# Kernel tuning notes

Measured on AMD Instinct MI355X. Metric: run time of the kernel, lower is better.

## Reference

```python
import jax, jax.numpy as jnp
import numpy as np

IN_DIM, HID, MID, FFN, OUT = 384, 128, 1024, 512, 1024
B, T = 8, 4096
LN_EPS = 1e-5


def _legs_hippo(n: int) -> np.ndarray:
    # A[i, j] = P_i(2j/n - 1) * sqrt(2i + 1), Legendre via 3-term recurrence
    x = 2.0 * np.arange(n) / n - 1.0          # eval points, shape [n]
    P = np.zeros((n, n), dtype=np.float64)     # P[i] = P_i(x)
    P[0] = 1.0
    if n > 1:
        P[1] = x
    for i in range(1, n - 1):
        P[i + 1] = ((2 * i + 1) * x * P[i] - i * P[i - 1]) / (i + 1)
    A = P * np.sqrt(2.0 * np.arange(n) + 1.0)[:, None]
    # rescale so the 4096-step recurrence stays finite (A is a free Parameter,
    # so any test value is valid; unscaled LegS overflows fp32 in ~20 steps)
    s = np.linalg.norm(A, 2)
    return (A / (1.05 * s)).astype(np.float32)


def _layernorm(x, g, b):
    mu = jnp.mean(x, axis=-1, keepdims=True)
    var = jnp.var(x, axis=-1, keepdims=True)
    return (x - mu) * jax.lax.rsqrt(var + LN_EPS) * g + b


def setup_inputs() -> dict:
    key = jax.random.key(0)
    ks = jax.random.split(key, 16)

    def w(k, shape, fan_in):
        return jax.random.normal(k, shape, jnp.float32) * (1.0 / np.sqrt(fan_in))

    return {
        "padded_x": jax.random.normal(ks[0], (B, T, IN_DIM), jnp.float32),
        "seq_lens": jax.random.randint(ks[1], (B,), 1, T + 1, jnp.int32),
        "A": jnp.asarray(_legs_hippo(HID)),
        "enc_w1": w(ks[2], (IN_DIM, MID), IN_DIM), "enc_b1": jnp.zeros((MID,), jnp.float32),
        "enc_w2": w(ks[3], (MID, HID), MID), "enc_b2": jnp.zeros((HID,), jnp.float32),
        "proj_w": w(ks[4], (HID, MID), HID), "proj_b": jnp.zeros((MID,), jnp.float32),
        "ln1_g": jnp.ones((MID,), jnp.float32), "ln1_b": jnp.zeros((MID,), jnp.float32),
        "ffn_w1": w(ks[5], (MID, FFN), MID), "ffn_b1": jnp.zeros((FFN,), jnp.float32),
        "ffn_w2": w(ks[6], (FFN, OUT), FFN), "ffn_b2": jnp.zeros((OUT,), jnp.float32),
        "ln2_g": jnp.ones((OUT,), jnp.float32), "ln2_b": jnp.zeros((OUT,), jnp.float32),
        "out_w": w(ks[7], (OUT, OUT), OUT), "out_b": jnp.zeros((OUT,), jnp.float32),
    }


def reference(padded_x, seq_lens, A, enc_w1, enc_b1, enc_w2, enc_b2,
              proj_w, proj_b, ln1_g, ln1_b, ffn_w1, ffn_b1, ffn_w2, ffn_b2,
              ln2_g, ln2_b, out_w, out_b):
    # encoder: Linear -> GELU(exact) -> Linear   [B, T, HID]
    h_mid = jax.nn.gelu(padded_x @ enc_w1 + enc_b1, approximate=False)
    seqs_bx = h_mid @ enc_w2 + enc_b2

    # masked linear recurrence h_t = A @ h_{t-1} + Bx_t via lax.scan over time
    xs = jnp.swapaxes(seqs_bx, 0, 1)           # [T, B, HID]
    ts = jnp.arange(xs.shape[0])

    def step(h, inp):
        x_t, t = inp
        upd = h @ A.T + x_t                     # (A @ h)^T batched
        mask = (t < seq_lens)[:, None]          # [B, 1]
        return jnp.where(mask, upd, h), None

    h0 = jnp.zeros((padded_x.shape[0], A.shape[0]), padded_x.dtype)
    batch_h, _ = jax.lax.scan(step, h0, (xs, ts))

    # decoder
    projected = batch_h @ proj_w + proj_b
    norm_h = _layernorm(projected, ln1_g, ln1_b)
    ffn_out = jax.nn.gelu(norm_h @ ffn_w1 + ffn_b1, approximate=False) @ ffn_w2 + ffn_b2
    ffn_out = ffn_out + projected               # residual (requires OUT == MID)
    norm_ffn = _layernorm(ffn_out, ln2_g, ln2_b)
    return norm_ffn @ out_w + out_b             # [B, OUT]
```

## Files before the change

kernel.cpp:

```cpp
#include <hip/hip_runtime.h>

typedef __attribute__((ext_vector_type(8))) short short8;
typedef __attribute__((ext_vector_type(4))) short short4v;
typedef __attribute__((ext_vector_type(4))) float float4v;

__device__ __forceinline__ float bf2f(short s) {
  union { float f; unsigned u; } cv; cv.u = ((unsigned)(unsigned short)s) << 16; return cv.f;
}
__device__ __forceinline__ short f2bf(float f) {
  union { float f; unsigned u; } cv; cv.f = f;
  unsigned u = cv.u;
  unsigned r = u + 0x7FFFu + ((u >> 16) & 1u);
  return (short)(r >> 16);
}
__device__ __forceinline__ float gelu_f(float v) {
  float ax = fabsf(v) * 0.70710678118654752440f;
  float t = __builtin_amdgcn_rcpf(__builtin_fmaf(0.3275911f, ax, 1.0f));
  float poly = __builtin_fmaf(t, 1.061405429f, -1.453152027f);
  poly = __builtin_fmaf(t, poly, 1.421413741f);
  poly = __builtin_fmaf(t, poly, -0.284496736f);
  poly = __builtin_fmaf(t, poly, 0.254829592f);
  poly *= t;
  float e = __expf(-ax * ax);
  float erfax = __builtin_fmaf(-poly, e, 1.0f);
  float erfx = (v < 0.0f) ? -erfax : erfax;
  return 0.5f * v * (1.0f + erfx);
}
__device__ __forceinline__ void glds16(const short* g, short* l) {
  __builtin_amdgcn_global_load_lds(
      (const __attribute__((address_space(1))) void*)g,
      (__attribute__((address_space(3))) void*)l, 16, 0, 0);
}

__device__ __forceinline__ void mm128(const short* __restrict__ P, const short* __restrict__ Qt,
                                      int mode, short* __restrict__ R,
                                      int table1, int slot,
                                      short* __restrict__ P1, short* __restrict__ P1t,
                                      short* __restrict__ P2t)
{
  int t = threadIdx.x, lane = t & 63, wave = t >> 6;
  int l15 = lane & 15, quad = lane >> 4;
#pragma unroll 1
  for (int p = 0; p < 2; ++p) {
    float4v acc[8];
#pragma unroll
    for (int nt = 0; nt < 8; ++nt) acc[nt] = 0;
#pragma unroll 1
    for (int ks = 0; ks < 4; ++ks) {
      short8 af = *(const short8*)&P[(wave * 32 + p * 16 + l15) * 128 + ks * 32 + quad * 8];
#pragma unroll
      for (int nt = 0; nt < 8; ++nt) {
        short8 bf = *(const short8*)&Qt[(nt * 16 + l15) * 128 + ks * 32 + quad * 8];
        acc[nt] = __builtin_amdgcn_mfma_f32_16x16x32_bf16(af, bf, acc[nt], 0, 0, 0);
      }
    }
    int mb = wave * 32 + p * 16 + quad * 4;
#pragma unroll
    for (int nt = 0; nt < 8; ++nt) {
      int n = nt * 16 + l15;
      short4v o;
#pragma unroll
      for (int reg = 0; reg < 4; ++reg) o[reg] = f2bf(acc[nt][reg]);
      if (mode == 2) {
        if (table1) {
#pragma unroll
          for (int reg = 0; reg < 4; ++reg) P1[(size_t)(mb + reg) * 8192 + slot * 128 + n] = o[reg];
          *(short4v*)&P1t[((size_t)slot * 128 + n) * 128 + mb] = o;
        } else {
          *(short4v*)&P2t[((size_t)slot * 128 + n) * 128 + mb] = o;
        }
      } else {
#pragma unroll
        for (int reg = 0; reg < 4; ++reg) R[(mb + reg) * 128 + n] = o[reg];
      }
    }
  }
  __syncthreads();
}

__global__ __launch_bounds__(256) void enc_fused(
    const short* __restrict__ xB, const short* __restrict__ w1T,
    const short* __restrict__ w2T, const float* __restrict__ b1,
    float* __restrict__ encP, const int* __restrict__ seq_lens,
    short* __restrict__ Spow, short* __restrict__ SpowT)
{
  __shared__ __align__(16) short lds[20480];
  int tid = threadIdx.x, lane = tid & 63, wave = tid >> 6;
  int l15 = lane & 15, quad = lane >> 4;

  if (blockIdx.x >= 512) {
    if (blockIdx.x != 512 || blockIdx.y != 0) return;
    short* XTl = lds;
    for (int i = tid * 8; i < 16384; i += 2048) {
      short8 v = *(const short8*)&SpowT[i];
      int row = i >> 7, seg = (i & 127) >> 3;
      int sw = (seg & 8) | ((seg & 7) ^ (row & 7));
      *(short8*)&XTl[row * 128 + sw * 8] = v;
    }
    __syncthreads();
    for (int step = 1; step <= 11; ++step) {
      const short* gX = Spow + (size_t)(step - 1) * 16384;
      short* gXo  = Spow  + (size_t)step * 16384;
      short* gXTo = SpowT + (size_t)step * 16384;
      short4v outs[2][8];
#pragma unroll 1
      for (int p = 0; p < 2; ++p) {
        int row = wave * 32 + p * 16 + l15;
        short8 af[4];
#pragma unroll
        for (int ks = 0; ks < 4; ++ks)
          af[ks] = *(const short8*)&gX[row * 128 + ks * 32 + quad * 8];
        float4v acc[8];
#pragma unroll
        for (int nt = 0; nt < 8; ++nt) acc[nt] = 0;
#pragma unroll
        for (int ks = 0; ks < 4; ++ks) {
          int seg = ks * 4 + quad;
#pragma unroll
          for (int nt = 0; nt < 8; ++nt) {
            int br = nt * 16 + l15;
            int sw = (seg & 8) | ((seg & 7) ^ (br & 7));
            short8 bf = *(const short8*)&XTl[br * 128 + sw * 8];
            acc[nt] = __builtin_amdgcn_mfma_f32_16x16x32_bf16(af[ks], bf, acc[nt], 0, 0, 0);
          }
        }
        int mb = wave * 32 + p * 16 + quad * 4;
#pragma unroll
        for (int nt = 0; nt < 8; ++nt) {
          int n = nt * 16 + l15;
          short4v o;
#pragma unroll
          for (int reg = 0; reg < 4; ++reg) {
            o[reg] = f2bf(acc[nt][reg]);
            gXo[(mb + reg) * 128 + n] = o[reg];
          }
          *(short4v*)&gXTo[(size_t)n * 128 + mb] = o;
          outs[p][nt] = o;
        }
      }
      __syncthreads();
#pragma unroll
      for (int p = 0; p < 2; ++p) {
        int mb = wave * 32 + p * 16 + quad * 4;
#pragma unroll
        for (int nt = 0; nt < 8; ++nt) {
          int n = nt * 16 + l15;
          int seg = mb >> 3;
          int sw = (seg & 8) | ((seg & 7) ^ (n & 7));
          *(short4v*)&XTl[n * 128 + sw * 8 + (mb & 7)] = outs[p][nt];
        }
      }
      __syncthreads();
    }
    return;
  }

  int m0 = blockIdx.x * 64;
  { int b = m0 >> 12, t = m0 & 4095; if (t >= seq_lens[b]) return; }
  int nc0 = blockIdx.y * 2;

  short* As   = lds;
  short* Ws   = lds + 4096;
  short* midb = lds + 12288;

  int lr = lane >> 3, lseg = lane & 7;

  float4v accO[4][2];
#pragma unroll
  for (int i = 0; i < 4; i++)
#pragma unroll
    for (int j = 0; j < 2; j++) accO[i][j] = 0;

  for (int nci = 0; nci < 2; ++nci) {
    int nc = nc0 + nci;
    float4v accM[4][2];
#pragma unroll
    for (int i = 0; i < 4; i++)
#pragma unroll
      for (int j = 0; j < 2; j++) accM[i][j] = 0;

    for (int ks = 0; ks < 6; ++ks) {
      int kk = ks * 64;
#pragma unroll
      for (int i = 0; i < 2; i++) {
        int rowg = wave * 16 + i * 8;
        glds16(xB + (size_t)(m0 + rowg + lr) * 384 + kk + (lseg ^ lr) * 8, &As[rowg * 64]);
      }
#pragma unroll
      for (int i = 0; i < 4; i++) {
        int rowg = wave * 32 + i * 8;
        glds16(w1T + (size_t)(nc * 128 + rowg + lr) * 384 + kk + (lseg ^ lr) * 8, &Ws[rowg * 64]);
      }
      __syncthreads();
#pragma unroll
      for (int kh = 0; kh < 2; kh++) {
        int s = kh * 4 + quad;
        short8 af[4], bfr[2];
#pragma unroll
        for (int im = 0; im < 4; im++) {
          int r = im * 16 + l15;
          af[im] = *(short8*)&As[r * 64 + ((s ^ (r & 7)) * 8)];
        }
#pragma unroll
        for (int in = 0; in < 2; in++) {
          int r = wave * 32 + in * 16 + l15;
          bfr[in] = *(short8*)&Ws[r * 64 + ((s ^ (r & 7)) * 8)];
        }
#pragma unroll
        for (int im = 0; im < 4; im++)
#pragma unroll
          for (int in = 0; in < 2; in++)
            accM[im][in] = __builtin_amdgcn_mfma_f32_16x16x32_bf16(af[im], bfr[in], accM[im][in], 0, 0, 0);
      }
      __syncthreads();
    }
#pragma unroll
    for (int in = 0; in < 2; in++) {
      int k = wave * 32 + in * 16 + l15;
      float bias = b1[nc * 128 + k];
      int s = k >> 3, kb = k & 7;
#pragma unroll
      for (int im = 0; im < 4; im++)
#pragma unroll
        for (int reg = 0; reg < 4; reg++) {
          int m = im * 16 + quad * 4 + reg;
          float v = gelu_f(accM[im][in][reg] + bias);
          int sw = (s & 8) | ((s & 7) ^ (m & 7));
          midb[m * 128 + sw * 8 + kb] = f2bf(v);
        }
    }
    __syncthreads();
#pragma unroll
    for (int ks2 = 0; ks2 < 2; ++ks2) {
      int kk = nc * 128 + ks2 * 64;
#pragma unroll
      for (int i = 0; i < 4; i++) {
        int rowg = wave * 32 + i * 8;
        glds16(w2T + (size_t)(rowg + lr) * 1024 + kk + (lseg ^ lr) * 8, &Ws[rowg * 64]);
      }
      __syncthreads();
#pragma unroll
      for (int kh = 0; kh < 2; kh++) {
        short8 af[4], bfr[2];
#pragma unroll
        for (int im = 0; im < 4; im++) {
          int m = im * 16 + l15;
          int kb = ks2 * 64 + kh * 32 + quad * 8;
          int s = kb >> 3;
          int sw = (s & 8) | ((s & 7) ^ (m & 7));
          af[im] = *(short8*)&midb[m * 128 + sw * 8];
        }
#pragma unroll
        for (int in = 0; in < 2; in++) {
          int r = wave * 32 + in * 16 + l15;
          int s = kh * 4 + quad;
          bfr[in] = *(short8*)&Ws[r * 64 + ((s ^ (r & 7)) * 8)];
        }
#pragma unroll
        for (int im = 0; im < 4; im++)
#pragma unroll
          for (int in = 0; in < 2; in++)
            accO[im][in] = __builtin_amdgcn_mfma_f32_16x16x32_bf16(af[im], bfr[in], accO[im][in], 0, 0, 0);
      }
      __syncthreads();
    }
  }
  float* outp = encP + ((size_t)blockIdx.y << 22);
#pragma unroll
  for (int im = 0; im < 4; im++)
#pragma unroll
    for (int in = 0; in < 2; in++) {
      int n = wave * 32 + in * 16 + l15;
#pragma unroll
      for (int reg = 0; reg < 4; reg++) {
        int m = m0 + im * 16 + quad * 4 + reg;
        outp[(size_t)m * 128 + n] = accO[im][in][reg];
      }
    }
}

__global__ __launch_bounds__(256) void enc_reduce(
    const float* __restrict__ encP, const float* __restrict__ b2,
    short* __restrict__ seqs, const int* __restrict__ seq_lens,
    const short* __restrict__ Spow, const short* __restrict__ SpowT,
    short* __restrict__ P1, short* __restrict__ P1t, short* __restrict__ P2t,
    short* __restrict__ powScr)
{
  if (blockIdx.x >= 512) {
    int bid = blockIdx.x - 512;
    int table1 = bid < 63 ? 1 : 0;
    int e = table1 ? bid + 1 : bid - 62;
    int slot = 63 - e;
    int bits = e;
    int k0 = __ffs(bits) - 1; bits &= bits - 1;
    int s0 = table1 ? k0 : (k0 == 0 ? 6 : 6 + k0);
    const short* cur = Spow + (size_t)s0 * 16384;
    short* scr = powScr + (size_t)bid * 2 * 16384;
    int sb = 0;
    if (!bits) {
      int t = threadIdx.x;
      for (int idx = t * 8; idx < 16384; idx += 2048) {
        short8 v = *(const short8*)&cur[idx];
        int i = idx >> 7, j0 = idx & 127;
        if (table1) {
          *(short8*)&P1[(size_t)i * 8192 + slot * 128 + j0] = v;
#pragma unroll
          for (int q = 0; q < 8; ++q) P1t[((size_t)slot * 128 + j0 + q) * 128 + i] = v[q];
        } else {
#pragma unroll
          for (int q = 0; q < 8; ++q) P2t[((size_t)slot * 128 + j0 + q) * 128 + i] = v[q];
        }
      }
      return;
    }
    while (true) {
      int k = __ffs(bits) - 1; bits &= bits - 1;
      int si = table1 ? k : (k == 0 ? 6 : 6 + k);
      const short* Bt = SpowT + (size_t)si * 16384;
      if (!bits) {
        mm128(cur, Bt, 2, nullptr, table1, slot, P1, P1t, P2t);
        return;
      }
      mm128(cur, Bt, 1, scr + sb * 16384, 0, 0, nullptr, nullptr, nullptr);
      cur = scr + sb * 16384; sb ^= 1;
    }
  }

  int m0 = blockIdx.x * 64;
  { int b = m0 >> 12, t = m0 & 4095; if (t >= seq_lens[b]) return; }
  int t = threadIdx.x;
#pragma unroll
  for (int i = 0; i < 8; i++) {
    int f4 = t + i * 256;
    int m = m0 + (f4 >> 5);
    int cg = f4 & 31;
    size_t off = (size_t)m * 128 + cg * 4;
    float4v v = *(const float4v*)&encP[off];
#pragma unroll
    for (int y = 1; y < 4; y++) {
      float4v w = *(const float4v*)&encP[((size_t)y << 22) + off];
#pragma unroll
      for (int q = 0; q < 4; q++) v[q] += w[q];
    }
    float4v bb = *(const float4v*)&b2[cg * 4];
    short4v o;
#pragma unroll
    for (int q = 0; q < 4; q++) o[q] = f2bf(v[q] + bb[q]);
    *(short4v*)&seqs[off] = o;
  }
}

__global__ __launch_bounds__(256) void gemm_bt(
    const short* __restrict__ A_, const short* __restrict__ BT,
    float* __restrict__ out, int lda, int ldb, int ldc,
    int kSteps, int kChunk)
{
  int m0 = blockIdx.y * 128;
  int n0 = blockIdx.x * 128;
  int kBase = blockIdx.z * kChunk;

  __shared__ __align__(16) short As[128 * 64];
  __shared__ __align__(16) short Bs[128 * 64];

  int tid = threadIdx.x;
  int lane = tid & 63, wave = tid >> 6;
  int l15 = lane & 15, quad = lane >> 4;
  int wm = wave & 1, wn = wave >> 1;
  int lr = lane >> 3, lseg = lane & 7;

  float4v acc[4][4];
#pragma unroll
  for (int i = 0; i < 4; i++)
#pragma unroll
    for (int j = 0; j < 4; j++) acc[i][j] = 0;

  for (int ks = 0; ks < kSteps; ++ks) {
    int kk = kBase + ks * 64;
#pragma unroll
    for (int i = 0; i < 4; i++) {
      int rowg = wave * 32 + i * 8;
      glds16(A_ + (size_t)(m0 + rowg + lr) * lda + kk + (lseg ^ lr) * 8, &As[rowg * 64]);
      glds16(BT + (size_t)(n0 + rowg + lr) * ldb + kk + (lseg ^ lr) * 8, &Bs[rowg * 64]);
    }
    __syncthreads();
#pragma unroll
    for (int kh = 0; kh < 2; kh++) {
      int s = kh * 4 + quad;
      short8 af[4], bfr[4];
#pragma unroll
      for (int im = 0; im < 4; im++) {
        int r = wm * 64 + im * 16 + l15;
        af[im] = *(short8*)&As[r * 64 + ((s ^ (r & 7)) * 8)];
      }
#pragma unroll
      for (int in = 0; in < 4; in++) {
        int r = wn * 64 + in * 16 + l15;
        bfr[in] = *(short8*)&Bs[r * 64 + ((s ^ (r & 7)) * 8)];
      }
#pragma unroll
      for (int im = 0; im < 4; im++)
#pragma unroll
        for (int in = 0; in < 4; in++)
          acc[im][in] = __builtin_amdgcn_mfma_f32_16x16x32_bf16(af[im], bfr[in], acc[im][in], 0, 0, 0);
    }
    __syncthreads();
  }
  float* outz = out + (size_t)blockIdx.z * 65536;
#pragma unroll
  for (int im = 0; im < 4; im++)
#pragma unroll
    for (int in = 0; in < 4; in++) {
      int n = n0 + wn * 64 + in * 16 + l15;
#pragma unroll
      for (int reg = 0; reg < 4; reg++) {
        int m = m0 + wm * 64 + im * 16 + quad * 4 + reg;
        outz[(size_t)m * ldc + n] = acc[im][in][reg];
      }
    }
}

__global__ void prep_wide(const float* __restrict__ x, const float* __restrict__ w1,
                          const float* __restrict__ w2,
                          const float* __restrict__ proj_w, const float* __restrict__ ffn_w1,
                          const float* __restrict__ ffn_w2, const float* __restrict__ out_w,
                          const float* __restrict__ A, const int* __restrict__ seq_lens,
                          short* __restrict__ xB,
                          short* __restrict__ w1T, short* __restrict__ w2T,
                          short* __restrict__ projB, short* __restrict__ ffn1B,
                          short* __restrict__ ffn2B, short* __restrict__ outB,
                          short* __restrict__ P1, short* __restrict__ P1t,
                          short* __restrict__ P2t,
                          short* __restrict__ Spow, short* __restrict__ SpowT)
{
  int idx = blockIdx.x * 256 + threadIdx.x;
  if (idx < 3145728) {
    int row = idx / 96;
    int t = row & 4095, b = row >> 12;
    if (t >= seq_lens[b]) return;
    float4v v = ((const float4v*)x)[idx];
    short4v o;
#pragma unroll
    for (int j = 0; j < 4; j++) o[j] = f2bf(v[j]);
    ((short4v*)xB)[idx] = o;
    return;
  }
  idx -= 3145728;
  if (idx < 393216) {
    int n = idx / 384, k = idx % 384;
    w1T[idx] = f2bf(w1[k * 1024 + n]);
    return;
  }
  idx -= 393216;
  if (idx < 131072) {
    int n = idx / 1024, k = idx % 1024;
    w2T[idx] = f2bf(w2[k * 128 + n]);
    return;
  }
  idx -= 131072;
  if (idx < 131072) { projB[idx] = f2bf(proj_w[idx]); return; }
  idx -= 131072;
  if (idx < 524288) { ffn1B[idx] = f2bf(ffn_w1[idx]); return; }
  idx -= 524288;
  if (idx < 524288) { ffn2B[idx] = f2bf(ffn_w2[idx]); return; }
  idx -= 524288;
  if (idx < 1048576) { outB[idx] = f2bf(out_w[idx]); return; }
  idx -= 1048576;
  if (idx < 16384) {
    int i = idx >> 7, j = idx & 127;
    short bidv = f2bf((i == j) ? 1.0f : 0.0f);
    P1[i * 8192 + 63 * 128 + j] = bidv;
    P1t[(63 * 128 + j) * 128 + i] = bidv;
    P2t[(63 * 128 + j) * 128 + i] = bidv;
    short ab = f2bf(A[idx]);
    Spow[idx] = ab;
    SpowT[(size_t)j * 128 + i] = ab;
  }
}

__global__ __launch_bounds__(256) void combine_gemm(
    const float* __restrict__ Vz, const short* __restrict__ seqs,
    const int* __restrict__ seq_lens,
    const short* __restrict__ P2t, const short* __restrict__ P1t,
    float* __restrict__ hFtail)
{
  __shared__ short X[256 * 8];
  int pp = blockIdx.x >> 5, ks = blockIdx.x & 31;
  int t = threadIdx.x;
  for (int e = t; e < 2048; e += 256) {
    int klocal = e >> 3, b = e & 7;
    int cp = ks * 2 + (klocal >> 7), i = klocal & 127;
    int L = seq_lens[b];
    if (pp == 0) {
      int F = L >> 6, sh = 64 - F;
      float v = 0.f;
      if (cp >= sh) {
        int row = (b * 64 + (cp - sh)) * 128 + i;
#pragma unroll
        for (int z = 0; z < 32; z++) v += Vz[(size_t)z * 65536 + row];
      }
      X[e] = f2bf(v);
    } else {
      int F = L >> 6, rr = L & 63, sh = 64 - rr;
      short s = 0;
      if (cp >= sh) s = seqs[((size_t)b * 4096 + F * 64 + (cp - sh)) * 128 + i];
      X[e] = s;
    }
  }
  __syncthreads();
  const short* P = pp ? P1t : P2t;
  float* outp = hFtail + pp * 1024;
  int i = t & 127, g = t >> 7;
  float acc[4] = {0, 0, 0, 0};
  for (int kl = 0; kl < 256; ++kl) {
    int k = ks * 256 + kl;
    float pv = bf2f(P[k * 128 + i]);
    short4v xv = *(const short4v*)(X + kl * 8 + g * 4);
#pragma unroll
    for (int q = 0; q < 4; q++) acc[q] += bf2f(xv[q]) * pv;
  }
#pragma unroll
  for (int q = 0; q < 4; q++) atomicAdd(&outp[(g * 4 + q) * 128 + i], acc[q]);
}

__global__ __launch_bounds__(256) void proj_stage(
    const float* __restrict__ hFtail, const short* __restrict__ P1t,
    const int* __restrict__ seq_lens, const short* __restrict__ projB,
    const float* __restrict__ proj_b, float* __restrict__ projected)
{
  __shared__ short hT[128 * 8];
  __shared__ float red[4][64][8];
  int t = threadIdx.x;
  {
    int b = t >> 5, i4 = (t & 31) * 4;
    int rr = seq_lens[b] & 63;
    const short* M = P1t + (size_t)(63 - rr) * 128 * 128;
    const float* hF = hFtail + b * 128;
    float acc[4];
#pragma unroll
    for (int q = 0; q < 4; q++) acc[q] = hFtail[1024 + b * 128 + i4 + q];
    for (int j = 0; j < 128; ++j) {
      float hv = hF[j];
      short4v mv = *(const short4v*)&M[j * 128 + i4];
#pragma unroll
      for (int q = 0; q < 4; q++) acc[q] += bf2f(mv[q]) * hv;
    }
#pragma unroll
    for (int q = 0; q < 4; q++) hT[(i4 + q) * 8 + b] = f2bf(acc[q]);
  }
  __syncthreads();
  int c = t & 63, sl = t >> 6;
  int n = blockIdx.x * 64 + c;
  float acc[8] = {0, 0, 0, 0, 0, 0, 0, 0};
  for (int k = sl * 32; k < sl * 32 + 32; ++k) {
    short8 xv = *(short8*)&hT[k * 8];
    float wv = bf2f(projB[k * 1024 + n]);
#pragma unroll
    for (int b = 0; b < 8; b++) acc[b] += bf2f(xv[b]) * wv;
  }
#pragma unroll
  for (int b = 0; b < 8; b++) red[sl][c][b] = acc[b];
  __syncthreads();
  if (sl == 0) {
#pragma unroll
    for (int s = 1; s < 4; s++)
#pragma unroll
      for (int b = 0; b < 8; b++) acc[b] += red[s][c][b];
    float bn = proj_b[n];
#pragma unroll
    for (int b = 0; b < 8; b++) projected[b * 1024 + n] = acc[b] + bn;
  }
}

__global__ __launch_bounds__(256) void ffn1_stage(
    const float* __restrict__ projected, const float* __restrict__ g1,
    const float* __restrict__ b1, const short* __restrict__ ffn1B,
    float* __restrict__ ffn1raw)
{
  __shared__ float part[8][32][2];
  __shared__ float stats[8][2];
  __shared__ short xT[256 * 8];
  __shared__ float red[4][64][8];
  int t = threadIdx.x;
  { int b = t >> 5, j0 = t & 31; float s = 0, q = 0;
    for (int k = j0 * 32; k < j0 * 32 + 32; ++k) { float v = projected[b * 1024 + k]; s += v; q += v * v; }
    part[b][j0][0] = s; part[b][j0][1] = q; }
  __syncthreads();
  if (t < 8) {
    float s = 0, q = 0;
    for (int j = 0; j < 32; j++) { s += part[t][j][0]; q += part[t][j][1]; }
    float mu = s * (1.0f / 1024.0f);
    float var = q * (1.0f / 1024.0f) - mu * mu;
    stats[t][0] = mu; stats[t][1] = rsqrtf(var + 1e-5f);
  }
  __syncthreads();
  int ky0 = blockIdx.y * 256;
  for (int idx = t; idx < 2048; idx += 256) {
    int kl = idx >> 3, b = idx & 7; int k = ky0 + kl;
    float v = (projected[b * 1024 + k] - stats[b][0]) * stats[b][1] * g1[k] + b1[k];
    xT[kl * 8 + b] = f2bf(v);
  }
  __syncthreads();
  int c = t & 63, sl = t >> 6;
  int n = blockIdx.x * 64 + c;
  float acc[8] = {0, 0, 0, 0, 0, 0, 0, 0};
  for (int kl = sl * 64; kl < sl * 64 + 64; ++kl) {
    short8 xv = *(short8*)&xT[kl * 8];
    float wv = bf2f(ffn1B[(size_t)(ky0 + kl) * 512 + n]);
#pragma unroll
    for (int b = 0; b < 8; b++) acc[b] += bf2f(xv[b]) * wv;
  }
#pragma unroll
  for (int b = 0; b < 8; b++) red[sl][c][b] = acc[b];
  __syncthreads();
  if (sl == 0) {
#pragma unroll
    for (int s = 1; s < 4; s++)
#pragma unroll
      for (int b = 0; b < 8; b++) acc[b] += red[s][c][b];
#pragma unroll
    for (int b = 0; b < 8; b++) atomicAdd(&ffn1raw[b * 512 + n], acc[b]);
  }
}

__global__ __launch_bounds__(256) void ffn2_stage(
    const float* __restrict__ ffn1raw, const float* __restrict__ fb1,
    const short* __restrict__ ffn2B, float* __restrict__ ffn2raw)
{
  __shared__ short xT[256 * 8];
  __shared__ float red[4][64][8];
  int t = threadIdx.x;
  int ky0 = blockIdx.y * 256;
  for (int idx = t; idx < 2048; idx += 256) {
    int kl = idx >> 3, b = idx & 7; int k = ky0 + kl;
    float v = gelu_f(ffn1raw[b * 512 + k] + fb1[k]);
    xT[kl * 8 + b] = f2bf(v);
  }
  __syncthreads();
  int c = t & 63, sl = t >> 6;
  int n = blockIdx.x * 64 + c;
  float acc[8] = {0, 0, 0, 0, 0, 0, 0, 0};
  for (int kl = sl * 64; kl < sl * 64 + 64; ++kl) {
    short8 xv = *(short8*)&xT[kl * 8];
    float wv = bf2f(ffn2B[(size_t)(ky0 + kl) * 1024 + n]);
#pragma unroll
    for (int b = 0; b < 8; b++) acc[b] += bf2f(xv[b]) * wv;
  }
#pragma unroll
  for (int b = 0; b < 8; b++) red[sl][c][b] = acc[b];
  __syncthreads();
  if (sl == 0) {
#pragma unroll
    for (int s = 1; s < 4; s++)
#pragma unroll
      for (int b = 0; b < 8; b++) acc[b] += red[s][c][b];
#pragma unroll
    for (int b = 0; b < 8; b++) atomicAdd(&ffn2raw[b * 1024 + n], acc[b]);
  }
}

__global__ __launch_bounds__(256) void out_stage(
    const float* __restrict__ ffn2raw, const float* __restrict__ fb2,
    const float* __restrict__ projected, const float* __restrict__ g2,
    const float* __restrict__ b2ln, const short* __restrict__ outB,
    const float* __restrict__ out_b, float* __restrict__ d_out)
{
  __shared__ float part[8][32][2];
  __shared__ float stats[8][2];
  __shared__ short xT[512 * 8];
  __shared__ float red[4][64][8];
  int t = threadIdx.x;
  { int b = t >> 5, j0 = t & 31; float s = 0, q = 0;
    for (int k = j0 * 32; k < j0 * 32 + 32; ++k) {
      float v = ffn2raw[b * 1024 + k] + fb2[k] + projected[b * 1024 + k];
      s += v; q += v * v;
    }
    part[b][j0][0] = s; part[b][j0][1] = q; }
  __syncthreads();
  if (t < 8) {
    float s = 0, q = 0;
    for (int j = 0; j < 32; j++) { s += part[t][j][0]; q += part[t][j][1]; }
    float mu = s * (1.0f / 1024.0f);
    float var = q * (1.0f / 1024.0f) - mu * mu;
    stats[t][0] = mu; stats[t][1] = rsqrtf(var + 1e-5f);
  }
  __syncthreads();
  int ky0 = blockIdx.y * 512;
  for (int idx = t; idx < 4096; idx += 256) {
    int kl = idx >> 3, b = idx & 7; int k = ky0 + kl;
    float v = ffn2raw[b * 1024 + k] + fb2[k] + projected[b * 1024 + k];
    v = (v - stats[b][0]) * stats[b][1] * g2[k] + b2ln[k];
    xT[kl * 8 + b] = f2bf(v);
  }
  __syncthreads();
  int c = t & 63, sl = t >> 6;
  int n = blockIdx.x * 64 + c;
  float acc[8] = {0, 0, 0, 0, 0, 0, 0, 0};
  for (int kl = sl * 128; kl < sl * 128 + 128; ++kl) {
    short8 xv = *(short8*)&xT[kl * 8];
    float wv = bf2f(outB[(size_t)(ky0 + kl) * 1024 + n]);
#pragma unroll
    for (int b = 0; b < 8; b++) acc[b] += bf2f(xv[b]) * wv;
  }
#pragma unroll
  for (int b = 0; b < 8; b++) red[sl][c][b] = acc[b];
  __syncthreads();
  if (sl == 0) {
#pragma unroll
    for (int s = 1; s < 4; s++)
#pragma unroll
      for (int b = 0; b < 8; b++) acc[b] += red[s][c][b];
    float bn = (blockIdx.y == 0) ? out_b[n] : 0.0f;
#pragma unroll
    for (int b = 0; b < 8; b++) atomicAdd(&d_out[b * 1024 + n], acc[b] + bn);
  }
}

extern "C" void kernel_launch(void* const* d_in, const int* in_sizes, int n_in,
                              void* d_out, int out_size, void* d_ws, size_t ws_size,
                              hipStream_t stream)
{
  (void)in_sizes; (void)n_in; (void)out_size; (void)ws_size;
  const float* x      = (const float*)d_in[0];
  const int* seq_lens = (const int*)d_in[1];
  const float* A      = (const float*)d_in[2];
  const float* enc_w1 = (const float*)d_in[3];
  const float* enc_b1 = (const float*)d_in[4];
  const float* enc_w2 = (const float*)d_in[5];
  const float* enc_b2 = (const float*)d_in[6];
  const float* proj_w = (const float*)d_in[7];
  const float* proj_b = (const float*)d_in[8];
  const float* ln1_g  = (const float*)d_in[9];
  const float* ln1_b  = (const float*)d_in[10];
  const float* ffn_w1 = (const float*)d_in[11];
  const float* ffn_b1 = (const float*)d_in[12];
  const float* ffn_w2 = (const float*)d_in[13];
  const float* ffn_b2 = (const float*)d_in[14];
  const float* ln2_g  = (const float*)d_in[15];
  const float* ln2_b  = (const float*)d_in[16];
  const float* out_w  = (const float*)d_in[17];
  const float* out_b  = (const float*)d_in[18];

  char* p = (char*)d_ws;
  auto alloc = [&](size_t bytes) { char* r = p; p += (bytes + 255) & ~(size_t)255; return r; };
  short* xB    = (short*)alloc(32768ull * 384 * 2);
  float* encP  = (float*)alloc(4ull * 32768 * 128 * 4);
  short* seqs  = (short*)alloc(32768ull * 128 * 2);
  short* w1T   = (short*)alloc(1024ull * 384 * 2);
  short* w2T   = (short*)alloc(128ull * 1024 * 2);
  short* projB = (short*)alloc(128ull * 1024 * 2);
  short* ffn1B = (short*)alloc(1024ull * 512 * 2);
  short* ffn2B = (short*)alloc(512ull * 1024 * 2);
  short* outB  = (short*)alloc(1024ull * 1024 * 2);
  short* Spow  = (short*)alloc(12ull * 16384 * 2);
  short* SpowT = (short*)alloc(12ull * 16384 * 2);
  short* P1    = (short*)alloc(128ull * 8192 * 2);
  short* P1t   = (short*)alloc(8192ull * 128 * 2);
  short* P2t   = (short*)alloc(8192ull * 128 * 2);
  short* powScr= (short*)alloc(126ull * 2 * 16384 * 2);
  float* Vz    = (float*)alloc(32ull * 512 * 128 * 4);
  float* hFtail  = (float*)alloc(2ull * 8 * 128 * 4);
  float* ffn1raw = (float*)alloc(8ull * 512 * 4);
  float* ffn2raw = (float*)alloc(8ull * 1024 * 4);
  float* projected = (float*)alloc(8ull * 1024 * 4);

  hipMemsetAsync(hFtail, 0, (2ull * 8 * 128 + 8ull * 512 + 8ull * 1024) * 4, stream);
  hipMemsetAsync(d_out, 0, 8192ull * 4, stream);

  prep_wide<<<23104, 256, 0, stream>>>(x, enc_w1, enc_w2, proj_w, ffn_w1, ffn_w2, out_w, A,
      seq_lens, xB, w1T, w2T, projB, ffn1B, ffn2B, outB, P1, P1t, P2t, Spow, SpowT);

  enc_fused<<<dim3(520, 4), 256, 0, stream>>>(xB, w1T, w2T, enc_b1, encP, seq_lens, Spow, SpowT);
  enc_reduce<<<638, 256, 0, stream>>>(encP, enc_b2, seqs, seq_lens, Spow, SpowT,
      P1, P1t, P2t, powScr);

  gemm_bt<<<dim3(1, 4, 32), 256, 0, stream>>>(seqs, P1, Vz, 8192, 8192, 128, 4, 256);
  combine_gemm<<<64, 256, 0, stream>>>(Vz, seqs, seq_lens, P2t, P1t, hFtail);

  proj_stage<<<16, 256, 0, stream>>>(hFtail, P1t, seq_lens, projB, proj_b, projected);
  ffn1_stage<<<dim3(8, 4), 256, 0, stream>>>(projected, ln1_g, ln1_b, ffn1B, ffn1raw);
  ffn2_stage<<<dim3(16, 2), 256, 0, stream>>>(ffn1raw, ffn_b1, ffn2B, ffn2raw);
  out_stage<<<dim3(16, 2), 256, 0, stream>>>(ffn2raw, ffn_b2, projected, ln2_g, ln2_b,
      outB, out_b, (float*)d_out);
}
```

Measured before the change: 368.5 us.

## Shrink encoder LDS, raise priority of power chain, fold memsets into prep kernel

The encoder kernel's LDS drops from 40KB to 32KB by staging the GELU intermediate in two 64-column halves, and launch bounds now request 5 waves per EU, both aimed at higher occupancy. The serial matrix-power chain block now reads its A operand from LDS instead of global memory, reloads the transposed result from global after each step, and runs at raised wave priority, as do the power blocks in enc_reduce, to shorten the critical path. The two hipMemsetAsync calls are folded into extra blocks of prep_wide to save launches, and mm128 hoists its A-fragment loads out of the k loop. Risks include register spills under the tighter launch bound and extra global round-trips per power step.

```diff
diff --git a/kernel.cpp b/kernel.cpp
--- a/kernel.cpp
+++ b/kernel.cpp
@@ -42,16 +42,19 @@
   int l15 = lane & 15, quad = lane >> 4;
 #pragma unroll 1
   for (int p = 0; p < 2; ++p) {
+    short8 af[4];
+#pragma unroll
+    for (int ks = 0; ks < 4; ++ks)
+      af[ks] = *(const short8*)&P[(wave * 32 + p * 16 + l15) * 128 + ks * 32 + quad * 8];
     float4v acc[8];
 #pragma unroll
     for (int nt = 0; nt < 8; ++nt) acc[nt] = 0;
 #pragma unroll 1
     for (int ks = 0; ks < 4; ++ks) {
-      short8 af = *(const short8*)&P[(wave * 32 + p * 16 + l15) * 128 + ks * 32 + quad * 8];
 #pragma unroll
       for (int nt = 0; nt < 8; ++nt) {
         short8 bf = *(const short8*)&Qt[(nt * 16 + l15) * 128 + ks * 32 + quad * 8];
-        acc[nt] = __builtin_amdgcn_mfma_f32_16x16x32_bf16(af, bf, acc[nt], 0, 0, 0);
+        acc[nt] = __builtin_amdgcn_mfma_f32_16x16x32_bf16(af[ks], bf, acc[nt], 0, 0, 0);
       }
     }
     int mb = wave * 32 + p * 16 + quad * 4;
@@ -78,38 +81,44 @@
   __syncthreads();
 }
 
-__global__ __launch_bounds__(256) void enc_fused(
+__global__ __launch_bounds__(256, 5) void enc_fused(
     const short* __restrict__ xB, const short* __restrict__ w1T,
     const short* __restrict__ w2T, const float* __restrict__ b1,
     float* __restrict__ encP, const int* __restrict__ seq_lens,
     short* __restrict__ Spow, short* __restrict__ SpowT)
 {
-  __shared__ __align__(16) short lds[20480];
+  __shared__ __align__(16) short lds[16384];
   int tid = threadIdx.x, lane = tid & 63, wave = tid >> 6;
   int l15 = lane & 15, quad = lane >> 4;
 
   if (blockIdx.x >= 512) {
     if (blockIdx.x != 512 || blockIdx.y != 0) return;
+    __builtin_amdgcn_s_setprio(1);
     short* XTl = lds;
     for (int i = tid * 8; i < 16384; i += 2048) {
       short8 v = *(const short8*)&SpowT[i];
-      int row = i >> 7, seg = (i & 127) >> 3;
-      int sw = (seg & 8) | ((seg & 7) ^ (row & 7));
-      *(short8*)&XTl[row * 128 + sw * 8] = v;
+      int c = i >> 7, seg = (i & 127) >> 3;
+      int sw = (seg & 8) | ((seg & 7) ^ (c & 7));
+      *(short8*)&XTl[c * 128 + sw * 8] = v;
     }
     __syncthreads();
     for (int step = 1; step <= 11; ++step) {
-      const short* gX = Spow + (size_t)(step - 1) * 16384;
       short* gXo  = Spow  + (size_t)step * 16384;
       short* gXTo = SpowT + (size_t)step * 16384;
-      short4v outs[2][8];
 #pragma unroll 1
       for (int p = 0; p < 2; ++p) {
         int row = wave * 32 + p * 16 + l15;
+        int rs = row >> 3, r7 = row & 7;
         short8 af[4];
 #pragma unroll
-        for (int ks = 0; ks < 4; ++ks)
-          af[ks] = *(const short8*)&gX[row * 128 + ks * 32 + quad * 8];
+        for (int ks = 0; ks < 4; ++ks) {
+          int c0 = ks * 32 + quad * 8;
+#pragma unroll
+          for (int j = 0; j < 8; ++j) {
+            int sw = (rs & 8) | ((rs & 7) ^ (j & 7));
+            af[ks][j] = XTl[(c0 + j) * 128 + sw * 8 + r7];
+          }
+        }
         float4v acc[8];
 #pragma unroll
         for (int nt = 0; nt < 8; ++nt) acc[nt] = 0;
@@ -135,20 +144,14 @@
             gXo[(mb + reg) * 128 + n] = o[reg];
           }
           *(short4v*)&gXTo[(size_t)n * 128 + mb] = o;
-          outs[p][nt] = o;
         }
       }
       __syncthreads();
-#pragma unroll
-      for (int p = 0; p < 2; ++p) {
-        int mb = wave * 32 + p * 16 + quad * 4;
-#pragma unroll
-        for (int nt = 0; nt < 8; ++nt) {
-          int n = nt * 16 + l15;
-          int seg = mb >> 3;
-          int sw = (seg & 8) | ((seg & 7) ^ (n & 7));
-          *(short4v*)&XTl[n * 128 + sw * 8 + (mb & 7)] = outs[p][nt];
-        }
+      for (int i = tid * 8; i < 16384; i += 2048) {
+        short8 v = *(const short8*)&gXTo[i];
+        int c = i >> 7, seg = (i & 127) >> 3;
+        int sw = (seg & 8) | ((seg & 7) ^ (c & 7));
+        *(short8*)&XTl[c * 128 + sw * 8] = v;
       }
       __syncthreads();
     }
@@ -215,24 +218,26 @@
       __syncthreads();
     }
 #pragma unroll
-    for (int in = 0; in < 2; in++) {
-      int k = wave * 32 + in * 16 + l15;
-      float bias = b1[nc * 128 + k];
-      int s = k >> 3, kb = k & 7;
-#pragma unroll
-      for (int im = 0; im < 4; im++)
-#pragma unroll
-        for (int reg = 0; reg < 4; reg++) {
-          int m = im * 16 + quad * 4 + reg;
-          float v = gelu_f(accM[im][in][reg] + bias);
-          int sw = (s & 8) | ((s & 7) ^ (m & 7));
-          midb[m * 128 + sw * 8 + kb] = f2bf(v);
-        }
-    }
-    __syncthreads();
-#pragma unroll
     for (int ks2 = 0; ks2 < 2; ++ks2) {
       int kk = nc * 128 + ks2 * 64;
+      if ((wave >> 1) == ks2) {
+#pragma unroll
+        for (int in = 0; in < 2; in++) {
+          int k = wave * 32 + in * 16 + l15;
+          int kl = k - ks2 * 64;
+          float bias = b1[nc * 128 + k];
+          int s = kl >> 3, kb = kl & 7;
+#pragma unroll
+          for (int im = 0; im < 4; im++)
+#pragma unroll
+            for (int reg = 0; reg < 4; reg++) {
+              int m = im * 16 + quad * 4 + reg;
+              float v = gelu_f(accM[im][in][reg] + bias);
+              int sw = s ^ (m & 7);
+              midb[m * 64 + sw * 8 + kb] = f2bf(v);
+            }
+        }
+      }
 #pragma unroll
       for (int i = 0; i < 4; i++) {
         int rowg = wave * 32 + i * 8;
@@ -245,10 +250,9 @@
 #pragma unroll
         for (int im = 0; im < 4; im++) {
           int m = im * 16 + l15;
-          int kb = ks2 * 64 + kh * 32 + quad * 8;
-          int s = kb >> 3;
-          int sw = (s & 8) | ((s & 7) ^ (m & 7));
-          af[im] = *(short8*)&midb[m * 128 + sw * 8];
+          int kb = kh * 32 + quad * 8;
+          int sw = (kb >> 3) ^ (m & 7);
+          af[im] = *(short8*)&midb[m * 64 + sw * 8];
         }
 #pragma unroll
         for (int in = 0; in < 2; in++) {
@@ -287,6 +291,7 @@
     short* __restrict__ powScr)
 {
   if (blockIdx.x >= 512) {
+    __builtin_amdgcn_s_setprio(1);
     int bid = blockIdx.x - 512;
     int table1 = bid < 63 ? 1 : 0;
     int e = table1 ? bid + 1 : bid - 62;
@@ -430,7 +435,8 @@
                           short* __restrict__ ffn2B, short* __restrict__ outB,
                           short* __restrict__ P1, short* __restrict__ P1t,
                           short* __restrict__ P2t,
-                          short* __restrict__ Spow, short* __restrict__ SpowT)
+                          short* __restrict__ Spow, short* __restrict__ SpowT,
+                          float* __restrict__ zone, float* __restrict__ dout)
 {
   int idx = blockIdx.x * 256 + threadIdx.x;
   if (idx < 3145728) {
@@ -474,6 +480,18 @@
     short ab = f2bf(A[idx]);
     Spow[idx] = ab;
     SpowT[(size_t)j * 128 + i] = ab;
+    return;
+  }
+  idx -= 16384;
+  if (idx < 3584) {
+    float4v z = 0;
+    ((float4v*)zone)[idx] = z;
+    return;
+  }
+  idx -= 3584;
+  if (idx < 2048) {
+    float4v z = 0;
+    ((float4v*)dout)[idx] = z;
   }
 }
 
@@ -763,11 +781,9 @@
   float* ffn2raw = (float*)alloc(8ull * 1024 * 4);
   float* projected = (float*)alloc(8ull * 1024 * 4);
 
-  hipMemsetAsync(hFtail, 0, (2ull * 8 * 128 + 8ull * 512 + 8ull * 1024) * 4, stream);
-  hipMemsetAsync(d_out, 0, 8192ull * 4, stream);
-
-  prep_wide<<<23104, 256, 0, stream>>>(x, enc_w1, enc_w2, proj_w, ffn_w1, ffn_w2, out_w, A,
-      seq_lens, xB, w1T, w2T, projB, ffn1B, ffn2B, outB, P1, P1t, P2t, Spow, SpowT);
+  prep_wide<<<23126, 256, 0, stream>>>(x, enc_w1, enc_w2, proj_w, ffn_w1, ffn_w2, out_w, A,
+      seq_lens, xB, w1T, w2T, projB, ffn1B, ffn2B, outB, P1, P1t, P2t, Spow, SpowT,
+      hFtail, (float*)d_out);
 
   enc_fused<<<dim3(520, 4), 256, 0, stream>>>(xB, w1T, w2T, enc_b1, encP, seq_lens, Spow, SpowT);
   enc_reduce<<<638, 256, 0, stream>>>(encP, enc_b2, seqs, seq_lens, Spow, SpowT,
```

Result: slower. 545.2 us (+48.0%).
